# Kernel optimization log

Hardware: AMD Instinct MI355X
Metric: run time of the kernel (lower is better)

## Reference

```python
import jax, jax.numpy as jnp
import numpy as np

B, D, K = 131072, 64, 4096

def setup_inputs() -> dict:
    key = jax.random.key(0)
    k1, k2 = jax.random.split(key)
    z_e = jax.random.normal(k1, (B, D), dtype=jnp.float32)
    # nn.init.uniform_(-1/K, 1/K)
    codebook = jax.random.uniform(k2, (K, D), dtype=jnp.float32, minval=-1.0 / K, maxval=1.0 / K)
    return {"z_e": z_e, "codebook": codebook}

def reference(z_e, codebook):
    # squared-distance expansion: ||z||^2 + ||e||^2 - 2 z.e  -> (B, K)
    z2 = jnp.sum(z_e * z_e, axis=1, keepdims=True)          # (B, 1)
    e2 = jnp.sum(codebook * codebook, axis=1)[None, :]       # (1, K)
    ze = jnp.einsum('bd,kd->bk', z_e, codebook)              # (B, K)
    dist = z2 + e2 - 2.0 * ze
    codes = jnp.argmin(dist, axis=1)                         # (B,) int
    z_q = codebook[codes]                                    # (B, D) gather
    return (z_q, codes)
```

## Files before the change

kernel.cpp:

```cpp
#include <hip/hip_runtime.h>
#include <math.h>

#define Bn 131072
#define Dn 64
#define Kn 4096
#define TK 64
#define NKT (Kn / TK)

typedef _Float16 f16x8 __attribute__((ext_vector_type(8)));
typedef float f32x4 __attribute__((ext_vector_type(4)));

__device__ __forceinline__ unsigned umn(unsigned a, unsigned b) { return a < b ? a : b; }
__device__ __forceinline__ unsigned umx(unsigned a, unsigned b) { return a > b ? a : b; }

__global__ __launch_bounds__(256, 2) void vq_main(const float* __restrict__ z,
                                                  const float* __restrict__ cb,
                                                  float* __restrict__ out) {
  __shared__ __align__(16) unsigned char smem[33792];
  unsigned char* tb = smem;
  const int tid = threadIdx.x;
  const int lane = tid & 63;
  const int w = tid >> 6;
  const int q = lane >> 4;
  const int col = lane & 15;
  const int row0 = blockIdx.x * 256;

  f16x8 A[4][2];
#pragma unroll
  for (int i = 0; i < 4; ++i)
#pragma unroll
    for (int c = 0; c < 2; ++c) {
      const float* zp = z + (size_t)(row0 + w * 64 + i * 16 + col) * Dn + c * 32 + q * 8;
      float4 x0 = *(const float4*)zp;
      float4 x1 = *(const float4*)(zp + 4);
      f16x8 a;
      a[0] = (_Float16)(-2.f * x0.x); a[1] = (_Float16)(-2.f * x0.y);
      a[2] = (_Float16)(-2.f * x0.z); a[3] = (_Float16)(-2.f * x0.w);
      a[4] = (_Float16)(-2.f * x1.x); a[5] = (_Float16)(-2.f * x1.y);
      a[6] = (_Float16)(-2.f * x1.z); a[7] = (_Float16)(-2.f * x1.w);
      A[i][c] = a;
    }

  const int n = tid >> 2;
  const int p = tid & 3;
  const int wr0 = n * 128 + (((2 * p) ^ (n & 7)) << 4);
  const int wr1 = n * 128 + (((2 * p + 1) ^ (n & 7)) << 4);

  float4 pf0, pf1, pf2, pf3;
  {
    const float4* g = (const float4*)(cb + (size_t)n * Dn + p * 16);
    pf0 = g[0]; pf1 = g[1]; pf2 = g[2]; pf3 = g[3];
  }

  f32x4 acc[4][4];
  unsigned k1[4][4], k2[4][4];
#pragma unroll
  for (int i = 0; i < 4; ++i)
#pragma unroll
    for (int r = 0; r < 4; ++r) { k1[i][r] = 0xFFFFFFFFu; k2[i][r] = 0xFFFFFFFFu; }
  unsigned tg[4] = {0u, 1u, 2u, 3u};
  const f32x4 c256 = {256.f, 256.f, 256.f, 256.f};

  for (int kt = 0; kt < NKT; ++kt) {
    __syncthreads();
    float4 nf0 = pf0, nf1 = pf1, nf2 = pf2, nf3 = pf3;
    if (kt + 1 < NKT) {
      const float4* g = (const float4*)(cb + ((size_t)(kt + 1) * TK + n) * Dn + p * 16);
      pf0 = g[0]; pf1 = g[1]; pf2 = g[2]; pf3 = g[3];
    }
    {
      f16x8 h0, h1;
      h0[0] = (_Float16)(nf0.x * 4096.f); h0[1] = (_Float16)(nf0.y * 4096.f);
      h0[2] = (_Float16)(nf0.z * 4096.f); h0[3] = (_Float16)(nf0.w * 4096.f);
      h0[4] = (_Float16)(nf1.x * 4096.f); h0[5] = (_Float16)(nf1.y * 4096.f);
      h0[6] = (_Float16)(nf1.z * 4096.f); h0[7] = (_Float16)(nf1.w * 4096.f);
      h1[0] = (_Float16)(nf2.x * 4096.f); h1[1] = (_Float16)(nf2.y * 4096.f);
      h1[2] = (_Float16)(nf2.z * 4096.f); h1[3] = (_Float16)(nf2.w * 4096.f);
      h1[4] = (_Float16)(nf3.x * 4096.f); h1[5] = (_Float16)(nf3.y * 4096.f);
      h1[6] = (_Float16)(nf3.z * 4096.f); h1[7] = (_Float16)(nf3.w * 4096.f);
      *(f16x8*)(tb + wr0) = h0;
      *(f16x8*)(tb + wr1) = h1;
    }
    __syncthreads();

#pragma unroll
    for (int c = 0; c < 2; ++c)
#pragma unroll
      for (int t = 0; t < 4; ++t) {
        f16x8 Bf = *(const f16x8*)(tb + (t * 16 + col) * 128 + (((c * 4 + q) ^ (col & 7)) << 4));
#pragma unroll
        for (int i = 0; i < 4; ++i)
          acc[i][t] = __builtin_amdgcn_mfma_f32_16x16x32_f16(A[i][c], Bf,
                                                             (c == 0) ? c256 : acc[i][t], 0, 0, 0);
      }

#pragma unroll
    for (int i = 0; i < 4; ++i)
#pragma unroll
      for (int r = 0; r < 4; ++r) {
        unsigned K0 = (__float_as_uint(acc[i][0][r]) & 0xFFFFFF00u) | tg[0];
        unsigned K1v = (__float_as_uint(acc[i][1][r]) & 0xFFFFFF00u) | tg[1];
        unsigned K2v = (__float_as_uint(acc[i][2][r]) & 0xFFFFFF00u) | tg[2];
        unsigned K3v = (__float_as_uint(acc[i][3][r]) & 0xFFFFFF00u) | tg[3];
        unsigned lo = umn(K0, K1v), hi = umx(K0, K1v);
        k2[i][r] = umn(umn(k2[i][r], umx(k1[i][r], lo)), hi);
        k1[i][r] = umn(k1[i][r], lo);
        lo = umn(K2v, K3v); hi = umx(K2v, K3v);
        k2[i][r] = umn(umn(k2[i][r], umx(k1[i][r], lo)), hi);
        k1[i][r] = umn(k1[i][r], lo);
      }
#pragma unroll
    for (int t = 0; t < 4; ++t) tg[t] += 4;
  }

  __syncthreads();
  unsigned* dmp = (unsigned*)smem;
#pragma unroll
  for (int i = 0; i < 4; ++i)
#pragma unroll
    for (int r = 0; r < 4; ++r) {
      int rr = i * 16 + q * 4 + r;
      dmp[w * 2048 + rr * 32 + col * 2] = k1[i][r];
      dmp[w * 2048 + rr * 32 + col * 2 + 1] = k2[i][r];
    }
  __syncthreads();

  {
    const int r = tid;
    const unsigned* keys = dmp + (r >> 6) * 2048 + (r & 63) * 32;
    unsigned mk = 0xFFFFFFFFu;
    for (int cnd = 0; cnd < 32; ++cnd) mk = umn(mk, keys[cnd]);
    const float lim = __uint_as_float(mk & 0xFFFFFF00u) + 0.5f;

    const float4* zr4 = (const float4*)(z + (size_t)(row0 + r) * Dn);
    float4 zr[16];
#pragma unroll
    for (int g = 0; g < 16; ++g) zr[g] = zr4[g];

    float r8[8];
#pragma unroll
    for (int g = 0; g < 2; ++g) {
      float4 v = zr[g]; int j = g * 4;
      r8[j + 0] = __fmul_rn(v.x, v.x); r8[j + 1] = __fmul_rn(v.y, v.y);
      r8[j + 2] = __fmul_rn(v.z, v.z); r8[j + 3] = __fmul_rn(v.w, v.w);
    }
#pragma unroll
    for (int g = 2; g < 16; ++g) {
      float4 v = zr[g]; int j = (g & 1) * 4;
      r8[j + 0] = __fadd_rn(r8[j + 0], __fmul_rn(v.x, v.x));
      r8[j + 1] = __fadd_rn(r8[j + 1], __fmul_rn(v.y, v.y));
      r8[j + 2] = __fadd_rn(r8[j + 2], __fmul_rn(v.z, v.z));
      r8[j + 3] = __fadd_rn(r8[j + 3], __fmul_rn(v.w, v.w));
    }
    float z2f = __fadd_rn(__fadd_rn(__fadd_rn(r8[0], r8[1]), __fadd_rn(r8[2], r8[3])),
                          __fadd_rn(__fadd_rn(r8[4], r8[5]), __fadd_rn(r8[6], r8[7])));

    float bq = INFINITY; int bc = Kn;
    for (int cnd = 0; cnd < 32; ++cnd) {
      unsigned key = keys[cnd];
      float sc = __uint_as_float(key & 0xFFFFFF00u);
      if (sc > lim) continue;
      int tag = (int)(key & 0xFFu);
      int code = (tag >> 2) * 64 + (tag & 3) * 16 + (cnd >> 1);
      const float4* cr = (const float4*)(cb + (size_t)code * Dn);
      double ze = 0.0;
      float e8[8];
#pragma unroll
      for (int g = 0; g < 16; ++g) {
        float4 ev = cr[g]; float4 zv = zr[g];
        ze += (double)ev.x * (double)zv.x + (double)ev.y * (double)zv.y +
              (double)ev.z * (double)zv.z + (double)ev.w * (double)zv.w;
        int jj = (g & 1) * 4;
        if (g < 2) {
          e8[jj + 0] = __fmul_rn(ev.x, ev.x); e8[jj + 1] = __fmul_rn(ev.y, ev.y);
          e8[jj + 2] = __fmul_rn(ev.z, ev.z); e8[jj + 3] = __fmul_rn(ev.w, ev.w);
        } else {
          e8[jj + 0] = __fadd_rn(e8[jj + 0], __fmul_rn(ev.x, ev.x));
          e8[jj + 1] = __fadd_rn(e8[jj + 1], __fmul_rn(ev.y, ev.y));
          e8[jj + 2] = __fadd_rn(e8[jj + 2], __fmul_rn(ev.z, ev.z));
          e8[jj + 3] = __fadd_rn(e8[jj + 3], __fmul_rn(ev.w, ev.w));
        }
      }
      float e2f = __fadd_rn(__fadd_rn(__fadd_rn(e8[0], e8[1]), __fadd_rn(e8[2], e8[3])),
                            __fadd_rn(__fadd_rn(e8[4], e8[5]), __fadd_rn(e8[6], e8[7])));
      float zef = (float)ze;
      float t1 = __fadd_rn(z2f, e2f);
      float t2 = __fmul_rn(2.0f, zef);
      float qv = __fadd_rn(t1, -t2);
      if (qv < bq || (qv == bq && code < bc)) { bq = qv; bc = code; }
    }
    ((int*)(smem + 32768))[r] = bc;
    out[(size_t)Bn * Dn + row0 + r] = (float)bc;
  }
  __syncthreads();

  {
    const float4* cb4 = (const float4*)cb;
    float4* out4 = (float4*)out;
    const int* wc = (const int*)(smem + 32768);
#pragma unroll
    for (int i = 0; i < 16; ++i) {
      int t = i * 256 + tid;
      int r = t >> 4, c2 = t & 15;
      int wn = wc[r];
      out4[(size_t)(row0 + r) * 16 + c2] = cb4[(size_t)wn * 16 + c2];
    }
  }
}

extern "C" void kernel_launch(void* const* d_in, const int* in_sizes, int n_in,
                              void* d_out, int out_size, void* d_ws, size_t ws_size,
                              hipStream_t stream) {
  const float* z = (const float*)d_in[0];
  const float* cb = (const float*)d_in[1];
  float* out = (float*)d_out;
  vq_main<<<Bn / 256, 256, 0, stream>>>(z, cb, out);
}
```

Measured before the change: 221.6 us.

## Use 512-thread blocks with double-buffered codebook tiles and split rescoring

Doubles the threads per block so each wave handles 32 rows instead of 64, halving per-thread accumulator and key registers to allow more waves per CU. The codebook tile staging becomes double-buffered in LDS with a two-tile-ahead register prefetch, leaving one barrier per iteration instead of two. The exact fp64 rescoring is split across two threads per row, joined by a shuffle. The z row is no longer cached in registers during rescoring, so it is re-read from global memory for each candidate.

```diff
diff --git a/kernel.cpp b/kernel.cpp
--- a/kernel.cpp
+++ b/kernel.cpp
@@ -13,11 +13,12 @@
 __device__ __forceinline__ unsigned umn(unsigned a, unsigned b) { return a < b ? a : b; }
 __device__ __forceinline__ unsigned umx(unsigned a, unsigned b) { return a > b ? a : b; }
 
-__global__ __launch_bounds__(256, 2) void vq_main(const float* __restrict__ z,
+__global__ __launch_bounds__(512, 4) void vq_main(const float* __restrict__ z,
                                                   const float* __restrict__ cb,
                                                   float* __restrict__ out) {
-  __shared__ __align__(16) unsigned char smem[33792];
-  unsigned char* tb = smem;
+  __shared__ __align__(16) unsigned char smem[34816];
+  unsigned char* tb0 = smem;
+  unsigned char* tb1 = smem + 8192;
   const int tid = threadIdx.x;
   const int lane = tid & 63;
   const int w = tid >> 6;
@@ -25,12 +26,12 @@
   const int col = lane & 15;
   const int row0 = blockIdx.x * 256;
 
-  f16x8 A[4][2];
-#pragma unroll
-  for (int i = 0; i < 4; ++i)
+  f16x8 A[2][2];
+#pragma unroll
+  for (int i = 0; i < 2; ++i)
 #pragma unroll
     for (int c = 0; c < 2; ++c) {
-      const float* zp = z + (size_t)(row0 + w * 64 + i * 16 + col) * Dn + c * 32 + q * 8;
+      const float* zp = z + (size_t)(row0 + w * 32 + i * 16 + col) * Dn + c * 32 + q * 8;
       float4 x0 = *(const float4*)zp;
       float4 x1 = *(const float4*)(zp + 4);
       f16x8 a;
@@ -41,61 +42,63 @@
       A[i][c] = a;
     }
 
-  const int n = tid >> 2;
-  const int p = tid & 3;
-  const int wr0 = n * 128 + (((2 * p) ^ (n & 7)) << 4);
-  const int wr1 = n * 128 + (((2 * p + 1) ^ (n & 7)) << 4);
-
-  float4 pf0, pf1, pf2, pf3;
-  {
-    const float4* g = (const float4*)(cb + (size_t)n * Dn + p * 16);
-    pf0 = g[0]; pf1 = g[1]; pf2 = g[2]; pf3 = g[3];
-  }
-
-  f32x4 acc[4][4];
-  unsigned k1[4][4], k2[4][4];
-#pragma unroll
-  for (int i = 0; i < 4; ++i)
+  const int n = tid >> 3;
+  const int p = tid & 7;
+  const int wr = n * 128 + ((p ^ (n & 7)) << 4);
+
+  f32x4 acc[2][4];
+  unsigned k1[2][4], k2[2][4];
+#pragma unroll
+  for (int i = 0; i < 2; ++i)
 #pragma unroll
     for (int r = 0; r < 4; ++r) { k1[i][r] = 0xFFFFFFFFu; k2[i][r] = 0xFFFFFFFFu; }
   unsigned tg[4] = {0u, 1u, 2u, 3u};
   const f32x4 c256 = {256.f, 256.f, 256.f, 256.f};
 
+  float4 pf0, pf1;
+  {
+    const float4* g = (const float4*)(cb + (size_t)n * Dn + p * 8);
+    float4 c0 = g[0], c1 = g[1];
+    f16x8 h;
+    h[0] = (_Float16)(c0.x * 4096.f); h[1] = (_Float16)(c0.y * 4096.f);
+    h[2] = (_Float16)(c0.z * 4096.f); h[3] = (_Float16)(c0.w * 4096.f);
+    h[4] = (_Float16)(c1.x * 4096.f); h[5] = (_Float16)(c1.y * 4096.f);
+    h[6] = (_Float16)(c1.z * 4096.f); h[7] = (_Float16)(c1.w * 4096.f);
+    *(f16x8*)(tb0 + wr) = h;
+    const float4* g1 = (const float4*)(cb + (size_t)(TK + n) * Dn + p * 8);
+    pf0 = g1[0]; pf1 = g1[1];
+  }
+  __syncthreads();
+
   for (int kt = 0; kt < NKT; ++kt) {
-    __syncthreads();
-    float4 nf0 = pf0, nf1 = pf1, nf2 = pf2, nf3 = pf3;
+    unsigned char* tcur = (kt & 1) ? tb1 : tb0;
+    unsigned char* tnxt = (kt & 1) ? tb0 : tb1;
     if (kt + 1 < NKT) {
-      const float4* g = (const float4*)(cb + ((size_t)(kt + 1) * TK + n) * Dn + p * 16);
-      pf0 = g[0]; pf1 = g[1]; pf2 = g[2]; pf3 = g[3];
-    }
-    {
-      f16x8 h0, h1;
-      h0[0] = (_Float16)(nf0.x * 4096.f); h0[1] = (_Float16)(nf0.y * 4096.f);
-      h0[2] = (_Float16)(nf0.z * 4096.f); h0[3] = (_Float16)(nf0.w * 4096.f);
-      h0[4] = (_Float16)(nf1.x * 4096.f); h0[5] = (_Float16)(nf1.y * 4096.f);
-      h0[6] = (_Float16)(nf1.z * 4096.f); h0[7] = (_Float16)(nf1.w * 4096.f);
-      h1[0] = (_Float16)(nf2.x * 4096.f); h1[1] = (_Float16)(nf2.y * 4096.f);
-      h1[2] = (_Float16)(nf2.z * 4096.f); h1[3] = (_Float16)(nf2.w * 4096.f);
-      h1[4] = (_Float16)(nf3.x * 4096.f); h1[5] = (_Float16)(nf3.y * 4096.f);
-      h1[6] = (_Float16)(nf3.z * 4096.f); h1[7] = (_Float16)(nf3.w * 4096.f);
-      *(f16x8*)(tb + wr0) = h0;
-      *(f16x8*)(tb + wr1) = h1;
-    }
-    __syncthreads();
+      f16x8 h;
+      h[0] = (_Float16)(pf0.x * 4096.f); h[1] = (_Float16)(pf0.y * 4096.f);
+      h[2] = (_Float16)(pf0.z * 4096.f); h[3] = (_Float16)(pf0.w * 4096.f);
+      h[4] = (_Float16)(pf1.x * 4096.f); h[5] = (_Float16)(pf1.y * 4096.f);
+      h[6] = (_Float16)(pf1.z * 4096.f); h[7] = (_Float16)(pf1.w * 4096.f);
+      *(f16x8*)(tnxt + wr) = h;
+    }
+    if (kt + 2 < NKT) {
+      const float4* g = (const float4*)(cb + ((size_t)(kt + 2) * TK + n) * Dn + p * 8);
+      pf0 = g[0]; pf1 = g[1];
+    }
 
 #pragma unroll
     for (int c = 0; c < 2; ++c)
 #pragma unroll
       for (int t = 0; t < 4; ++t) {
-        f16x8 Bf = *(const f16x8*)(tb + (t * 16 + col) * 128 + (((c * 4 + q) ^ (col & 7)) << 4));
-#pragma unroll
-        for (int i = 0; i < 4; ++i)
+        f16x8 Bf = *(const f16x8*)(tcur + (t * 16 + col) * 128 + (((c * 4 + q) ^ (col & 7)) << 4));
+#pragma unroll
+        for (int i = 0; i < 2; ++i)
           acc[i][t] = __builtin_amdgcn_mfma_f32_16x16x32_f16(A[i][c], Bf,
                                                              (c == 0) ? c256 : acc[i][t], 0, 0, 0);
       }
 
 #pragma unroll
-    for (int i = 0; i < 4; ++i)
+    for (int i = 0; i < 2; ++i)
 #pragma unroll
       for (int r = 0; r < 4; ++r) {
         unsigned K0 = (__float_as_uint(acc[i][0][r]) & 0xFFFFFF00u) | tg[0];
@@ -111,42 +114,42 @@
       }
 #pragma unroll
     for (int t = 0; t < 4; ++t) tg[t] += 4;
-  }
-
-  __syncthreads();
+
+    __syncthreads();
+  }
+
   unsigned* dmp = (unsigned*)smem;
 #pragma unroll
-  for (int i = 0; i < 4; ++i)
+  for (int i = 0; i < 2; ++i)
 #pragma unroll
     for (int r = 0; r < 4; ++r) {
       int rr = i * 16 + q * 4 + r;
-      dmp[w * 2048 + rr * 32 + col * 2] = k1[i][r];
-      dmp[w * 2048 + rr * 32 + col * 2 + 1] = k2[i][r];
+      int rb = w * 32 + rr;
+      dmp[rb * 33 + col * 2] = k1[i][r];
+      dmp[rb * 33 + col * 2 + 1] = k2[i][r];
     }
   __syncthreads();
 
   {
-    const int r = tid;
-    const unsigned* keys = dmp + (r >> 6) * 2048 + (r & 63) * 32;
+    const int rl = tid >> 1;
+    const int half = tid & 1;
+    const unsigned* keys = dmp + rl * 33 + half * 16;
     unsigned mk = 0xFFFFFFFFu;
-    for (int cnd = 0; cnd < 32; ++cnd) mk = umn(mk, keys[cnd]);
+    for (int j = 0; j < 16; ++j) mk = umn(mk, keys[j]);
     const float lim = __uint_as_float(mk & 0xFFFFFF00u) + 0.5f;
 
-    const float4* zr4 = (const float4*)(z + (size_t)(row0 + r) * Dn);
-    float4 zr[16];
-#pragma unroll
-    for (int g = 0; g < 16; ++g) zr[g] = zr4[g];
+    const float4* zr4 = (const float4*)(z + (size_t)(row0 + rl) * Dn);
 
     float r8[8];
 #pragma unroll
     for (int g = 0; g < 2; ++g) {
-      float4 v = zr[g]; int j = g * 4;
+      float4 v = zr4[g]; int j = g * 4;
       r8[j + 0] = __fmul_rn(v.x, v.x); r8[j + 1] = __fmul_rn(v.y, v.y);
       r8[j + 2] = __fmul_rn(v.z, v.z); r8[j + 3] = __fmul_rn(v.w, v.w);
     }
 #pragma unroll
     for (int g = 2; g < 16; ++g) {
-      float4 v = zr[g]; int j = (g & 1) * 4;
+      float4 v = zr4[g]; int j = (g & 1) * 4;
       r8[j + 0] = __fadd_rn(r8[j + 0], __fmul_rn(v.x, v.x));
       r8[j + 1] = __fadd_rn(r8[j + 1], __fmul_rn(v.y, v.y));
       r8[j + 2] = __fadd_rn(r8[j + 2], __fmul_rn(v.z, v.z));
@@ -156,10 +159,11 @@
                           __fadd_rn(__fadd_rn(r8[4], r8[5]), __fadd_rn(r8[6], r8[7])));
 
     float bq = INFINITY; int bc = Kn;
-    for (int cnd = 0; cnd < 32; ++cnd) {
-      unsigned key = keys[cnd];
+    for (int j = 0; j < 16; ++j) {
+      unsigned key = keys[j];
       float sc = __uint_as_float(key & 0xFFFFFF00u);
       if (sc > lim) continue;
+      int cnd = half * 16 + j;
       int tag = (int)(key & 0xFFu);
       int code = (tag >> 2) * 64 + (tag & 3) * 16 + (cnd >> 1);
       const float4* cr = (const float4*)(cb + (size_t)code * Dn);
@@ -167,7 +171,7 @@
       float e8[8];
 #pragma unroll
       for (int g = 0; g < 16; ++g) {
-        float4 ev = cr[g]; float4 zv = zr[g];
+        float4 ev = cr[g]; float4 zv = zr4[g];
         ze += (double)ev.x * (double)zv.x + (double)ev.y * (double)zv.y +
               (double)ev.z * (double)zv.z + (double)ev.w * (double)zv.w;
         int jj = (g & 1) * 4;
@@ -189,18 +193,23 @@
       float qv = __fadd_rn(t1, -t2);
       if (qv < bq || (qv == bq && code < bc)) { bq = qv; bc = code; }
     }
-    ((int*)(smem + 32768))[r] = bc;
-    out[(size_t)Bn * Dn + row0 + r] = (float)bc;
+    float obq = __shfl_xor(bq, 1);
+    int obc = __shfl_xor(bc, 1);
+    if (obq < bq || (obq == bq && obc < bc)) { bq = obq; bc = obc; }
+    if (half == 0) {
+      ((int*)(smem + 33792))[rl] = bc;
+      out[(size_t)Bn * Dn + row0 + rl] = (float)bc;
+    }
   }
   __syncthreads();
 
   {
     const float4* cb4 = (const float4*)cb;
     float4* out4 = (float4*)out;
-    const int* wc = (const int*)(smem + 32768);
-#pragma unroll
-    for (int i = 0; i < 16; ++i) {
-      int t = i * 256 + tid;
+    const int* wc = (const int*)(smem + 33792);
+#pragma unroll
+    for (int i = 0; i < 8; ++i) {
+      int t = i * 512 + tid;
       int r = t >> 4, c2 = t & 15;
       int wn = wc[r];
       out4[(size_t)(row0 + r) * 16 + c2] = cb4[(size_t)wn * 16 + c2];
@@ -214,5 +223,5 @@
   const float* z = (const float*)d_in[0];
   const float* cb = (const float*)d_in[1];
   float* out = (float*)d_out;
-  vq_main<<<Bn / 256, 256, 0, stream>>>(z, cb, out);
+  vq_main<<<Bn / 256, 512, 0, stream>>>(z, cb, out);
 }
```

New measurement: 220.6 us. Within noise of the previous version (-0.5%).
